# Kernel optimization log

Measured on AMD Instinct MI355X. Metric: run time of the kernel, lower is better.

## Reference

```python
import jax, jax.numpy as jnp
import numpy as np

E = 8        # num_experts (== num_local_experts here)
H = 2048     # hidden_size
I = 1024     # intermediate_size
T = 8192     # num_tokens
K = 2        # top_k


def setup_inputs() -> dict:
    key = jax.random.key(0)
    ks = jax.random.split(key, 6)
    x = jax.random.normal(ks[0], (T, H), dtype=jnp.float32)
    selected_experts = jax.random.randint(ks[1], (T, K), 0, E, dtype=jnp.int32)
    routing_weights = jax.random.uniform(ks[2], (T, K), dtype=jnp.float32)
    # per-expert weights; torch Linear stores [out, in]; we store [E, in, out] for einsum
    gate_w = jax.random.normal(ks[3], (E, H, I), dtype=jnp.float32) * 0.02
    up_w = jax.random.normal(ks[4], (E, H, I), dtype=jnp.float32) * 0.02
    down_w = jax.random.normal(ks[5], (E, I, H), dtype=jnp.float32) * 0.02
    return {
        "x": x,
        "selected_experts": selected_experts,
        "routing_weights": routing_weights,
        "gate_w": gate_w,
        "up_w": up_w,
        "down_w": down_w,
    }


def reference(x, selected_experts, routing_weights, gate_w, up_w, down_w):
    # Combined per-(token, expert) weight: sum of routing weights over top-k slots
    # that selected this expert. Mathematically identical to the sort/dispatch/
    # weighted index_add_ in the original module.
    w = jnp.einsum(
        "tke,tk->te",
        jax.nn.one_hot(selected_experts, E, dtype=x.dtype),
        routing_weights.astype(x.dtype),
    )  # [T, E]
    g = jnp.einsum("th,ehi->eti", x, gate_w)               # [E, T, I]
    u = jnp.einsum("th,ehi->eti", x, up_w)                 # [E, T, I]
    a = jax.nn.gelu(g, approximate=True) * u               # gelu tanh approx
    # down-proj per expert then weighted combine (scatter-add equivalent)
    out = jnp.einsum("eti,eih,te->th", a, down_w, w)       # [T, H], float32
    return out
```

## Files before the change

### kernel.cpp

```cpp
#include <hip/hip_runtime.h>
#include <hip/hip_bf16.h>


typedef __attribute__((ext_vector_type(8))) short bf16x8;
typedef __attribute__((ext_vector_type(4))) float f32x4;
typedef __attribute__((ext_vector_type(4))) unsigned short us4;

#define AS1 __attribute__((address_space(1)))
#define AS3 __attribute__((address_space(3)))

static constexpr int T_TOK = 8192;
static constexpr int HID   = 2048;
static constexpr int INTER = 1024;
static constexpr int NEXP  = 8;
static constexpr int NPAIR = T_TOK * 2;
static constexpr int TM    = 256;
static constexpr int MAX_ROWS = NPAIR + NEXP * TM;
static constexpr int MAX_RT   = MAX_ROWS / TM;
static constexpr int OUTN = T_TOK * HID;

__device__ __forceinline__ unsigned short f2bf(float f) {
  unsigned u = __float_as_uint(f);
  u += 0x7fffu + ((u >> 16) & 1u);
  return (unsigned short)(u >> 16);
}
__device__ __forceinline__ float bf2f(unsigned short h) {
  return __uint_as_float(((unsigned)h) << 16);
}
__device__ __forceinline__ void glds16(const void* g, void* l) {
  __builtin_amdgcn_global_load_lds((const AS1 void*)g, (AS3 void*)l, 16, 0, 0);
}

__global__ void detect_k(const unsigned* __restrict__ xw, int* __restrict__ flagp) {
  int tid = threadIdx.x;
  int cnt = 0;
  for (int i = tid; i < 256; i += 64) {
    unsigned e = (xw[i] >> 7) & 0xffu;
    cnt += (e >= 0x70u && e <= 0x8fu) ? 1 : 0;
  }
  for (int off = 32; off; off >>= 1) cnt += __shfl_down(cnt, off);
  if (tid == 0) *flagp = (cnt >= 192) ? 1 : 0;
}

__global__ void zero_out_k(unsigned* __restrict__ out, const int* __restrict__ flagp) {
  int n = (*flagp) ? (OUTN / 2) : OUTN;
  int i = blockIdx.x * 256 + threadIdx.x;
  int stride = gridDim.x * 256;
  for (; i < n; i += stride) out[i] = 0u;
}

__global__ void routing_k(const int* __restrict__ sel, const void* __restrict__ rwv,
                          int* __restrict__ rows, float* __restrict__ wgt,
                          int* __restrict__ offs, int* __restrict__ pairpos,
                          const int* __restrict__ flagp) {
  __shared__ int cnt[NEXP], cur[NEXP], offs_s[NEXP + 1];
  int flag = *flagp;
  const unsigned short* rw16 = (const unsigned short*)rwv;
  const float* rwf = (const float*)rwv;
  int tid = threadIdx.x;
  if (tid < NEXP) cnt[tid] = 0;
  __syncthreads();
  for (int p = tid; p < NPAIR; p += 1024) atomicAdd(&cnt[sel[p]], 1);
  __syncthreads();
  if (tid == 0) {
    int off = 0;
    for (int e = 0; e < NEXP; ++e) {
      offs_s[e] = off; cur[e] = off;
      off += (cnt[e] + TM - 1) / TM * TM;
    }
    offs_s[NEXP] = off;
  }
  __syncthreads();
  if (tid <= NEXP) offs[tid] = offs_s[tid];
  for (int p = tid; p < NPAIR; p += 1024) {
    int e = sel[p];
    int pos = atomicAdd(&cur[e], 1);
    rows[pos] = p >> 1;
    wgt[pos] = flag ? bf2f(rw16[p]) : rwf[p];
    pairpos[p] = pos;
  }
  for (int e = 0; e < NEXP; ++e)
    for (int r = offs_s[e] + cnt[e] + tid; r < offs_s[e + 1]; r += 1024) {
      rows[r] = 0; wgt[r] = 0.f;
    }
}

__global__ void convert_x_k(const void* __restrict__ xin,
                            unsigned short* __restrict__ xc,
                            const int* __restrict__ flagp) {
  int flag = *flagp;
  const int nvec = (T_TOK * HID) / 8;
  int v = blockIdx.x * 256 + threadIdx.x;
  int stride = gridDim.x * 256;
  for (; v < nvec; v += stride) {
    if (flag) {
      ((uint4*)xc)[v] = ((const uint4*)xin)[v];
    } else {
      const float4* s = (const float4*)xin;
      float4 a = s[2 * v], b = s[2 * v + 1];
      uint4 o;
      o.x = (unsigned)f2bf(a.x) | ((unsigned)f2bf(a.y) << 16);
      o.y = (unsigned)f2bf(a.z) | ((unsigned)f2bf(a.w) << 16);
      o.z = (unsigned)f2bf(b.x) | ((unsigned)f2bf(b.y) << 16);
      o.w = (unsigned)f2bf(b.z) | ((unsigned)f2bf(b.w) << 16);
      ((uint4*)xc)[v] = o;
    }
  }
}

__global__ void transpose_k(const void* __restrict__ in,
                            unsigned short* __restrict__ out, int R, int C,
                            const int* __restrict__ flagp) {
  __shared__ unsigned short t[64 * 72];
  int flag = *flagp;
  int e = blockIdx.z;
  int c0 = blockIdx.x * 64, r0 = blockIdx.y * 64;
  int tid = threadIdx.x;
  int mr = tid >> 4;
  int mc = tid & 15;
  unsigned short b[4][4];
  if (flag) {
    const unsigned short* src = (const unsigned short*)in + (size_t)e * R * C;
#pragma unroll
    for (int i = 0; i < 4; ++i) {
      us4 v = *(const us4*)(src + (size_t)(r0 + mr * 4 + i) * C + c0 + mc * 4);
      b[i][0] = v[0]; b[i][1] = v[1]; b[i][2] = v[2]; b[i][3] = v[3];
    }
  } else {
    const float* src = (const float*)in + (size_t)e * R * C;
#pragma unroll
    for (int i = 0; i < 4; ++i) {
      float4 v = *(const float4*)(src + (size_t)(r0 + mr * 4 + i) * C + c0 + mc * 4);
      b[i][0] = f2bf(v.x); b[i][1] = f2bf(v.y); b[i][2] = f2bf(v.z); b[i][3] = f2bf(v.w);
    }
  }
#pragma unroll
  for (int j = 0; j < 4; ++j) {
    us4 w;
    w[0] = b[0][j]; w[1] = b[1][j]; w[2] = b[2][j]; w[3] = b[3][j];
    *(us4*)(&t[(mc * 4 + j) * 72 + mr * 4]) = w;
  }
  __syncthreads();
  int orow = tid >> 2, ch = (tid & 3) * 16;
  uint4 v0 = *(const uint4*)(&t[orow * 72 + ch]);
  uint4 v1 = *(const uint4*)(&t[orow * 72 + ch + 8]);
  unsigned short* dst = out + (size_t)e * R * C + (size_t)(c0 + orow) * R + r0 + ch;
  *(uint4*)(dst) = v0;
  *(uint4*)(dst + 8) = v1;
}


__device__ __forceinline__ const bf16x8* ldf(const unsigned short* sm, int slot,
                                             int r, int c8) {
  return (const bf16x8*)(sm + slot * 8192 + r * 64 + ((c8 ^ (r & 7)) << 3));
}
__device__ __forceinline__ void stage_half(const unsigned short* p0,
                                           const unsigned short* p1,
                                           unsigned short* dst) {
  glds16(p0, dst);
  glds16(p1, dst + 4096);
}

#define MFMA8(AH, BH, B)                                                       \
  _Pragma("unroll") for (int i_ = 0; i_ < 4; ++i_) {                           \
    _Pragma("unroll") for (int j_ = 0; j_ < 2; ++j_) {                         \
      acc[AH][BH][i_][j_] = __builtin_amdgcn_mfma_f32_16x16x32_bf16(           \
          a[i_][0], B[j_][0], acc[AH][BH][i_][j_], 0, 0, 0);                   \
      acc[AH][BH][i_][j_] = __builtin_amdgcn_mfma_f32_16x16x32_bf16(           \
          a[i_][1], B[j_][1], acc[AH][BH][i_][j_], 0, 0, 0);                   \
    }                                                                          \
  }

template <int BUF, bool S1, bool S2, int VM>
__device__ __forceinline__ void ktile(
    unsigned short* sm, int wbase, int rA, int rB, int lquad,
    const unsigned short* pA00, const unsigned short* pA01,
    const unsigned short* pA10, const unsigned short* pA11,
    const unsigned short* pB00, const unsigned short* pB01,
    const unsigned short* pB10, const unsigned short* pB11,
    int ko1, int ko2, f32x4 (&acc)[2][2][4][2]) {
  bf16x8 a[4][2], b0[2][2], b1[2][2];
#pragma unroll
  for (int i = 0; i < 4; ++i)
#pragma unroll
    for (int k = 0; k < 2; ++k)
      a[i][k] = *ldf(sm, BUF * 2 + 0, rA + i * 16, k * 4 + lquad);
#pragma unroll
  for (int j = 0; j < 2; ++j)
#pragma unroll
    for (int k = 0; k < 2; ++k)
      b0[j][k] = *ldf(sm, 4 + BUF * 2 + 0, rB + j * 16, k * 4 + lquad);
  if constexpr (S1)
    stage_half(pA10 + ko1, pA11 + ko1, sm + ((BUF ^ 1) * 2 + 1) * 8192 + wbase);
  __builtin_amdgcn_s_barrier();
  asm volatile("s_waitcnt lgkmcnt(0)" ::: "memory");
  __builtin_amdgcn_s_setprio(1);
  MFMA8(0, 0, b0);
  __builtin_amdgcn_s_setprio(0);
  __builtin_amdgcn_s_barrier();
#pragma unroll
  for (int j = 0; j < 2; ++j)
#pragma unroll
    for (int k = 0; k < 2; ++k)
      b1[j][k] = *ldf(sm, 4 + BUF * 2 + 1, rB + j * 16, k * 4 + lquad);
  if constexpr (S1)
    stage_half(pB00 + ko1, pB01 + ko1, sm + (4 + (BUF ^ 1) * 2 + 0) * 8192 + wbase);
  __builtin_amdgcn_s_barrier();
  asm volatile("s_waitcnt lgkmcnt(0)" ::: "memory");
  __builtin_amdgcn_s_setprio(1);
  MFMA8(0, 1, b1);
  __builtin_amdgcn_s_setprio(0);
  __builtin_amdgcn_s_barrier();
#pragma unroll
  for (int i = 0; i < 4; ++i)
#pragma unroll
    for (int k = 0; k < 2; ++k)
      a[i][k] = *ldf(sm, BUF * 2 + 1, rA + i * 16, k * 4 + lquad);
  if constexpr (S2)
    stage_half(pA00 + ko2, pA01 + ko2, sm + (BUF * 2 + 0) * 8192 + wbase);
  __builtin_amdgcn_s_barrier();
  asm volatile("s_waitcnt lgkmcnt(0)" ::: "memory");
  __builtin_amdgcn_s_setprio(1);
  MFMA8(1, 1, b1);
  __builtin_amdgcn_s_setprio(0);
  __builtin_amdgcn_s_barrier();
  if constexpr (S2)
    stage_half(pB10 + ko2, pB11 + ko2, sm + (4 + BUF * 2 + 1) * 8192 + wbase);
  __builtin_amdgcn_s_barrier();
  __builtin_amdgcn_s_setprio(1);
  MFMA8(1, 0, b0);
  __builtin_amdgcn_s_setprio(0);
  if constexpr (VM == 4)
    asm volatile("s_waitcnt vmcnt(4)" ::: "memory");
  else if constexpr (VM == 0)
    asm volatile("s_waitcnt vmcnt(0)" ::: "memory");
  __builtin_amdgcn_s_barrier();
}

__global__ __launch_bounds__(512, 2) void gemm_gateup8(
    const unsigned short* __restrict__ xc,
    const unsigned short* __restrict__ gwT,
    const unsigned short* __restrict__ uwT,
    const int* __restrict__ rows, const int* __restrict__ offs,
    unsigned short* __restrict__ act) {
  extern __shared__ unsigned short sm[];
  int nRT = offs[NEXP] >> 8;
  int rowTile = blockIdx.x >> 3;
  if (rowTile >= nRT) return;
  int nt = blockIdx.x & 7;
  int row0 = rowTile << 8;
  int e = 0;
  while (row0 >= offs[e + 1]) ++e;

  int tid = threadIdx.x;
  int lane = tid & 63, lrow = lane & 15, lquad = lane >> 4;
  int wave = tid >> 6;
  int wmg = wave >> 2, wng = wave & 3;
  int wbase = wave << 9;
  int rA = wmg * 64 + lrow;
  int rB = wng * 32 + lrow;

  int sr = tid >> 3;
  int swz = ((tid & 7) ^ (sr & 7)) << 3;

  const unsigned short* pA00 = xc + (size_t)rows[row0 + sr] * HID + swz;
  const unsigned short* pA01 = xc + (size_t)rows[row0 + 64 + sr] * HID + swz;
  const unsigned short* pA10 = xc + (size_t)rows[row0 + 128 + sr] * HID + swz;
  const unsigned short* pA11 = xc + (size_t)rows[row0 + 192 + sr] * HID + swz;
  const unsigned short* gB = gwT + ((size_t)e * INTER + (size_t)nt * 128) * HID;
  const unsigned short* uB = uwT + ((size_t)e * INTER + (size_t)nt * 128) * HID;
  const unsigned short* pB00 = gB + (size_t)sr * HID + swz;
  const unsigned short* pB01 = gB + (size_t)(64 + sr) * HID + swz;
  const unsigned short* pB10 = uB + (size_t)sr * HID + swz;
  const unsigned short* pB11 = uB + (size_t)(64 + sr) * HID + swz;

  f32x4 acc[2][2][4][2] = {};

  stage_half(pA00, pA01, sm + 0 * 8192 + wbase);
  stage_half(pB00, pB01, sm + 4 * 8192 + wbase);
  stage_half(pB10, pB11, sm + 5 * 8192 + wbase);
  stage_half(pA10, pA11, sm + 1 * 8192 + wbase);
  stage_half(pA00 + 64, pA01 + 64, sm + 2 * 8192 + wbase);
  stage_half(pB10 + 64, pB11 + 64, sm + 7 * 8192 + wbase);
  asm volatile("s_waitcnt vmcnt(4)" ::: "memory");
  __builtin_amdgcn_s_barrier();

  constexpr int NT = HID / 64;
#pragma unroll 1
  for (int it = 0; it < NT / 2 - 1; ++it) {
    int u = it * 2;
    ktile<0, true, true, 4>(sm, wbase, rA, rB, lquad, pA00, pA01, pA10, pA11,
                            pB00, pB01, pB10, pB11, (u + 1) * 64, (u + 2) * 64, acc);
    ktile<1, true, true, 4>(sm, wbase, rA, rB, lquad, pA00, pA01, pA10, pA11,
                            pB00, pB01, pB10, pB11, (u + 2) * 64, (u + 3) * 64, acc);
  }
  ktile<0, true, false, 0>(sm, wbase, rA, rB, lquad, pA00, pA01, pA10, pA11,
                           pB00, pB01, pB10, pB11, (NT - 1) * 64, 0, acc);
  ktile<1, false, false, -1>(sm, wbase, rA, rB, lquad, pA00, pA01, pA10, pA11,
                             pB00, pB01, pB10, pB11, 0, 0, acc);

  size_t actb = (size_t)row0 * INTER + (size_t)nt * 128 + wng * 32 + lrow;
#pragma unroll
  for (int ah = 0; ah < 2; ++ah)
#pragma unroll
    for (int i = 0; i < 4; ++i)
#pragma unroll
      for (int r = 0; r < 4; ++r) {
        int m = ah * 128 + wmg * 64 + i * 16 + lquad * 4 + r;
#pragma unroll
        for (int j = 0; j < 2; ++j) {
          float g = acc[ah][0][i][j][r], u = acc[ah][1][i][j][r];
          float z = 1.5957691f * (g + 0.044715f * g * g * g);
          float aout = g * u / (1.f + __expf(-z));
          act[actb + (size_t)m * INTER + j * 16] = f2bf(aout);
        }
      }
}

template <int EPI>
__global__ __launch_bounds__(512, 2) void gemm_down8(
    const unsigned short* __restrict__ act,
    const unsigned short* __restrict__ dwT,
    const int* __restrict__ rows, const float* __restrict__ wgt,
    const int* __restrict__ offs, void* __restrict__ outv,
    const int* __restrict__ flagp, float* __restrict__ y) {
  extern __shared__ unsigned short sm[];
  int nRT = offs[NEXP] >> 8;
  int rowTile = blockIdx.x >> 3;
  if (rowTile >= nRT) return;
  int nt = blockIdx.x & 7;
  int row0 = rowTile << 8;
  int e = 0;
  while (row0 >= offs[e + 1]) ++e;

  int tid = threadIdx.x;
  int lane = tid & 63, lrow = lane & 15, lquad = lane >> 4;
  int wave = tid >> 6;
  int wmg = wave >> 2, wng = wave & 3;
  int wbase = wave << 9;
  int rA = wmg * 64 + lrow;
  int rB = wng * 32 + lrow;

  int sr = tid >> 3;
  int swz = ((tid & 7) ^ (sr & 7)) << 3;

  const unsigned short* pA00 = act + (size_t)(row0 + sr) * INTER + swz;
  const unsigned short* pA01 = act + (size_t)(row0 + 64 + sr) * INTER + swz;
  const unsigned short* pA10 = act + (size_t)(row0 + 128 + sr) * INTER + swz;
  const unsigned short* pA11 = act + (size_t)(row0 + 192 + sr) * INTER + swz;
  const unsigned short* dB = dwT + ((size_t)e * HID + (size_t)nt * 256) * INTER;
  const unsigned short* pB00 = dB + (size_t)sr * INTER + swz;
  const unsigned short* pB01 = dB + (size_t)(64 + sr) * INTER + swz;
  const unsigned short* pB10 = dB + (size_t)(128 + sr) * INTER + swz;
  const unsigned short* pB11 = dB + (size_t)(192 + sr) * INTER + swz;

  f32x4 acc[2][2][4][2] = {};

  stage_half(pA00, pA01, sm + 0 * 8192 + wbase);
  stage_half(pB00, pB01, sm + 4 * 8192 + wbase);
  stage_half(pB10, pB11, sm + 5 * 8192 + wbase);
  stage_half(pA10, pA11, sm + 1 * 8192 + wbase);
  stage_half(pA00 + 64, pA01 + 64, sm + 2 * 8192 + wbase);
  stage_half(pB10 + 64, pB11 + 64, sm + 7 * 8192 + wbase);
  asm volatile("s_waitcnt vmcnt(4)" ::: "memory");
  __builtin_amdgcn_s_barrier();

  constexpr int NT = INTER / 64;
#pragma unroll 1
  for (int it = 0; it < NT / 2 - 1; ++it) {
    int u = it * 2;
    ktile<0, true, true, 4>(sm, wbase, rA, rB, lquad, pA00, pA01, pA10, pA11,
                            pB00, pB01, pB10, pB11, (u + 1) * 64, (u + 2) * 64, acc);
    ktile<1, true, true, 4>(sm, wbase, rA, rB, lquad, pA00, pA01, pA10, pA11,
                            pB00, pB01, pB10, pB11, (u + 2) * 64, (u + 3) * 64, acc);
  }
  ktile<0, true, false, 0>(sm, wbase, rA, rB, lquad, pA00, pA01, pA10, pA11,
                           pB00, pB01, pB10, pB11, (NT - 1) * 64, 0, acc);
  ktile<1, false, false, -1>(sm, wbase, rA, rB, lquad, pA00, pA01, pA10, pA11,
                             pB00, pB01, pB10, pB11, 0, 0, acc);

  if constexpr (EPI == 1) {
#pragma unroll
    for (int ah = 0; ah < 2; ++ah)
#pragma unroll
      for (int i = 0; i < 4; ++i)
#pragma unroll
        for (int r = 0; r < 4; ++r) {
          int m = row0 + ah * 128 + wmg * 64 + i * 16 + lquad * 4 + r;
          float w = wgt[m];
          float* yp = y + (size_t)m * HID + (size_t)nt * 256 + wng * 32 + lrow;
#pragma unroll
          for (int bh = 0; bh < 2; ++bh)
#pragma unroll
            for (int j = 0; j < 2; ++j)
              yp[bh * 128 + j * 16] = acc[ah][bh][i][j][r] * w;
        }
  } else {
    int flag = *flagp;
#pragma unroll
    for (int ah = 0; ah < 2; ++ah)
#pragma unroll
      for (int i = 0; i < 4; ++i)
#pragma unroll
        for (int r = 0; r < 4; ++r) {
          int m = row0 + ah * 128 + wmg * 64 + i * 16 + lquad * 4 + r;
          float w = wgt[m];
          int token = rows[m];
          size_t base = (size_t)token * HID + (size_t)nt * 256 + wng * 32 + lrow;
          if (flag) {
#pragma unroll
            for (int bh = 0; bh < 2; ++bh)
#pragma unroll
              for (int j = 0; j < 2; ++j) {
                float v = acc[ah][bh][i][j][r] * w;
                float o = __shfl_xor(v, 1);
                if (((lane & 1) == 0) && w != 0.f) {
                  unsigned* p = (unsigned*)((unsigned short*)outv + base + bh * 128 + j * 16);
                  unsigned old = __atomic_load_n(p, __ATOMIC_RELAXED), assumed;
                  do {
                    assumed = old;
                    float flo = bf2f((unsigned short)(assumed & 0xffffu));
                    float fhi = bf2f((unsigned short)(assumed >> 16));
                    unsigned nw = (unsigned)f2bf(flo + v) | ((unsigned)f2bf(fhi + o) << 16);
                    old = atomicCAS(p, assumed, nw);
                  } while (old != assumed);
                }
              }
          } else {
            if (w != 0.f) {
              float* outf = (float*)outv;
#pragma unroll
              for (int bh = 0; bh < 2; ++bh)
#pragma unroll
                for (int j = 0; j < 2; ++j)
                  atomicAdd(outf + base + bh * 128 + j * 16, acc[ah][bh][i][j][r] * w);
            }
          }
        }
  }
}

__global__ void combine_k(const float* __restrict__ y,
                          const int* __restrict__ pairpos,
                          void* __restrict__ outv, const int* __restrict__ flagp) {
  int flag = *flagp;
  const int NV = T_TOK * (HID / 4);
  int v = blockIdx.x * 256 + threadIdx.x;
  int stride = gridDim.x * 256;
  for (; v < NV; v += stride) {
    int t = v >> 9;
    int hq = (v & 511) * 4;
    int p0 = pairpos[2 * t], p1 = pairpos[2 * t + 1];
    float4 a = *(const float4*)(y + (size_t)p0 * HID + hq);
    float4 b = *(const float4*)(y + (size_t)p1 * HID + hq);
    float4 s;
    s.x = a.x + b.x; s.y = a.y + b.y; s.z = a.z + b.z; s.w = a.w + b.w;
    if (flag) {
      uint2 o;
      o.x = (unsigned)f2bf(s.x) | ((unsigned)f2bf(s.y) << 16);
      o.y = (unsigned)f2bf(s.z) | ((unsigned)f2bf(s.w) << 16);
      *(uint2*)((unsigned short*)outv + (size_t)v * 4) = o;
    } else {
      *(float4*)((float*)outv + (size_t)v * 4) = s;
    }
  }
}

extern "C" void kernel_launch(void* const* d_in, const int* in_sizes, int n_in,
                              void* d_out, int out_size, void* d_ws, size_t ws_size,
                              hipStream_t stream) {
  (void)in_sizes; (void)n_in; (void)out_size;
  const void* x   = d_in[0];
  const int* sel  = (const int*)d_in[1];
  const void* rw  = d_in[2];
  const void* gw  = d_in[3];
  const void* uw  = d_in[4];
  const void* dw  = d_in[5];

  char* ws = (char*)d_ws;
  int* offs     = (int*)ws;
  int* flagp    = (int*)(ws + 64);
  int* rows     = (int*)(ws + 256);
  float* wgt    = (float*)(ws + 256 + MAX_ROWS * 4);
  int* pairpos  = (int*)(ws + 256 + MAX_ROWS * 8);
  size_t off0   = 256 + (size_t)MAX_ROWS * 8 + (size_t)NPAIR * 4;
  off0 = (off0 + 255) & ~(size_t)255;
  unsigned short* dwT = (unsigned short*)(ws + off0);
  unsigned short* act = dwT + (size_t)NEXP * HID * INTER;
  unsigned short* gwT = act + (size_t)MAX_ROWS * INTER;
  unsigned short* uwT = gwT + (size_t)NEXP * HID * INTER;
  unsigned short* xc  = uwT + (size_t)NEXP * HID * INTER;
  float* y            = (float*)gwT;
  size_t y_end = ((char*)gwT - ws) + (size_t)MAX_ROWS * HID * 4;
  bool use_y = ws_size >= y_end;

  hipFuncSetAttribute(reinterpret_cast<const void*>(gemm_gateup8),
                      hipFuncAttributeMaxDynamicSharedMemorySize, 131072);
  hipFuncSetAttribute(reinterpret_cast<const void*>(gemm_down8<1>),
                      hipFuncAttributeMaxDynamicSharedMemorySize, 131072);
  hipFuncSetAttribute(reinterpret_cast<const void*>(gemm_down8<0>),
                      hipFuncAttributeMaxDynamicSharedMemorySize, 131072);

  detect_k<<<1, 64, 0, stream>>>((const unsigned*)x, flagp);
  if (!use_y)
    zero_out_k<<<4096, 256, 0, stream>>>((unsigned*)d_out, flagp);
  routing_k<<<1, 1024, 0, stream>>>(sel, rw, rows, wgt, offs, pairpos, flagp);
  transpose_k<<<dim3(INTER / 64, HID / 64, NEXP), 256, 0, stream>>>(gw, gwT, HID, INTER, flagp);
  transpose_k<<<dim3(INTER / 64, HID / 64, NEXP), 256, 0, stream>>>(uw, uwT, HID, INTER, flagp);
  transpose_k<<<dim3(HID / 64, INTER / 64, NEXP), 256, 0, stream>>>(dw, dwT, INTER, HID, flagp);
  convert_x_k<<<4096, 256, 0, stream>>>(x, xc, flagp);
  gemm_gateup8<<<MAX_RT * 8, 512, 131072, stream>>>(xc, gwT, uwT, rows, offs, act);
  if (use_y) {
    gemm_down8<1><<<MAX_RT * 8, 512, 131072, stream>>>(act, dwT, rows, wgt, offs,
                                                       d_out, flagp, y);
    combine_k<<<4096, 256, 0, stream>>>(y, pairpos, d_out, flagp);
  } else {
    gemm_down8<0><<<MAX_RT * 8, 512, 131072, stream>>>(act, dwT, rows, wgt, offs,
                                                       d_out, flagp, nullptr);
  }
}
```

Baseline: 583.1 us.

## Split single-block routing into multi-block count/offset/scatter kernels with wave-aggregated atomics

Replaces the one-block routing kernel with four kernels: a prefill that zeroes the rows and weights, a 32-block histogram using ballot-aggregated shared atomics, a tiny offset kernel, and a 32-block scatter that reserves slots with one global atomic per expert per wavefront. The goal is to spread the serial single-CU routing work over several CUs and cut atomic contention. In exchange it adds three kernel launches, and the order of rows within each expert now depends on scheduling.

```diff
diff --git a/kernel.cpp b/kernel.cpp
--- a/kernel.cpp
+++ b/kernel.cpp
@@ -49,40 +49,72 @@
   for (; i < n; i += stride) out[i] = 0u;
 }
 
-__global__ void routing_k(const int* __restrict__ sel, const void* __restrict__ rwv,
-                          int* __restrict__ rows, float* __restrict__ wgt,
-                          int* __restrict__ offs, int* __restrict__ pairpos,
-                          const int* __restrict__ flagp) {
-  __shared__ int cnt[NEXP], cur[NEXP], offs_s[NEXP + 1];
+__global__ void routing_prefill_k(int* __restrict__ rows, float* __restrict__ wgt,
+                                  int* __restrict__ cnt) {
+  int i = blockIdx.x * 256 + threadIdx.x;
+  if (i < NEXP) cnt[i] = 0;
+  for (; i < MAX_ROWS; i += gridDim.x * 256) { rows[i] = 0; wgt[i] = 0.f; }
+}
+
+__global__ void routing_count_k(const int* __restrict__ sel, int* __restrict__ cnt) {
+  __shared__ int lc[NEXP];
+  int tid = threadIdx.x;
+  int lane = tid & 63;
+  if (tid < NEXP) lc[tid] = 0;
+  __syncthreads();
+  for (int p = blockIdx.x * 256 + tid; p < NPAIR; p += 8192) {
+    int e = sel[p];
+#pragma unroll
+    for (int ee = 0; ee < NEXP; ++ee) {
+      unsigned long long m = __ballot(e == ee);
+      if (m && lane == __ffsll((long long)m) - 1)
+        atomicAdd(&lc[ee], (int)__popcll(m));
+    }
+  }
+  __syncthreads();
+  if (tid < NEXP) atomicAdd(&cnt[tid], lc[tid]);
+}
+
+__global__ void routing_offs_k(const int* __restrict__ cnt, int* __restrict__ offs,
+                               int* __restrict__ cur) {
+  if (threadIdx.x == 0) {
+    int off = 0;
+    for (int e = 0; e < NEXP; ++e) {
+      offs[e] = off; cur[e] = off;
+      off += (cnt[e] + TM - 1) / TM * TM;
+    }
+    offs[NEXP] = off;
+  }
+}
+
+__global__ void routing_scatter_k(const int* __restrict__ sel,
+                                  const void* __restrict__ rwv,
+                                  int* __restrict__ rows, float* __restrict__ wgt,
+                                  int* __restrict__ pairpos, int* __restrict__ cur,
+                                  const int* __restrict__ flagp) {
   int flag = *flagp;
   const unsigned short* rw16 = (const unsigned short*)rwv;
   const float* rwf = (const float*)rwv;
   int tid = threadIdx.x;
-  if (tid < NEXP) cnt[tid] = 0;
-  __syncthreads();
-  for (int p = tid; p < NPAIR; p += 1024) atomicAdd(&cnt[sel[p]], 1);
-  __syncthreads();
-  if (tid == 0) {
-    int off = 0;
-    for (int e = 0; e < NEXP; ++e) {
-      offs_s[e] = off; cur[e] = off;
-      off += (cnt[e] + TM - 1) / TM * TM;
-    }
-    offs_s[NEXP] = off;
-  }
-  __syncthreads();
-  if (tid <= NEXP) offs[tid] = offs_s[tid];
-  for (int p = tid; p < NPAIR; p += 1024) {
+  int lane = tid & 63;
+  for (int p = blockIdx.x * 256 + tid; p < NPAIR; p += 8192) {
     int e = sel[p];
-    int pos = atomicAdd(&cur[e], 1);
+    int pos = 0;
+#pragma unroll
+    for (int ee = 0; ee < NEXP; ++ee) {
+      unsigned long long m = __ballot(e == ee);
+      if (e == ee) {
+        int leader = __ffsll((long long)m) - 1;
+        int base = 0;
+        if (lane == leader) base = atomicAdd(&cur[ee], (int)__popcll(m));
+        base = __shfl(base, leader);
+        pos = base + (int)__popcll(m & ((1ull << lane) - 1ull));
+      }
+    }
     rows[pos] = p >> 1;
     wgt[pos] = flag ? bf2f(rw16[p]) : rwf[p];
     pairpos[p] = pos;
   }
-  for (int e = 0; e < NEXP; ++e)
-    for (int r = offs_s[e] + cnt[e] + tid; r < offs_s[e + 1]; r += 1024) {
-      rows[r] = 0; wgt[r] = 0.f;
-    }
 }
 
 __global__ void convert_x_k(const void* __restrict__ xin,
@@ -480,6 +512,8 @@
   char* ws = (char*)d_ws;
   int* offs     = (int*)ws;
   int* flagp    = (int*)(ws + 64);
+  int* cnt      = (int*)(ws + 128);
+  int* cur      = (int*)(ws + 160);
   int* rows     = (int*)(ws + 256);
   float* wgt    = (float*)(ws + 256 + MAX_ROWS * 4);
   int* pairpos  = (int*)(ws + 256 + MAX_ROWS * 8);
@@ -504,7 +538,10 @@
   detect_k<<<1, 64, 0, stream>>>((const unsigned*)x, flagp);
   if (!use_y)
     zero_out_k<<<4096, 256, 0, stream>>>((unsigned*)d_out, flagp);
-  routing_k<<<1, 1024, 0, stream>>>(sel, rw, rows, wgt, offs, pairpos, flagp);
+  routing_prefill_k<<<MAX_ROWS / 256, 256, 0, stream>>>(rows, wgt, cnt);
+  routing_count_k<<<32, 256, 0, stream>>>(sel, cnt);
+  routing_offs_k<<<1, 64, 0, stream>>>(cnt, offs, cur);
+  routing_scatter_k<<<32, 256, 0, stream>>>(sel, rw, rows, wgt, pairpos, cur, flagp);
   transpose_k<<<dim3(INTER / 64, HID / 64, NEXP), 256, 0, stream>>>(gw, gwT, HID, INTER, flagp);
   transpose_k<<<dim3(INTER / 64, HID / 64, NEXP), 256, 0, stream>>>(uw, uwT, HID, INTER, flagp);
   transpose_k<<<dim3(HID / 64, INTER / 64, NEXP), 256, 0, stream>>>(dw, dwT, INTER, HID, flagp);
```

Result: no change. 589.1 us (+1.0%).
